# Kernel optimization log

Measured on AMD Instinct MI355X. Metric: run time of the kernel, lower is better.

Reference implementation:

```python
import jax, jax.numpy as jnp
import numpy as np

EMB = 512
HEAD = 8
HEAD_DIM = EMB // HEAD


def setup_inputs() -> dict:
    key = jax.random.key(0)
    ks = jax.random.split(key, 12)
    B, S = 2, 4096
    scale = 1.0 / np.sqrt(EMB)
    inp = {
        "q": jax.random.normal(ks[0], (B, S, EMB), dtype=jnp.float32),
        "kv": jax.random.normal(ks[1], (B, S, EMB), dtype=jnp.float32),
        "Wq": jax.random.normal(ks[2], (EMB, EMB), dtype=jnp.float32) * scale,
        "bq": jax.random.normal(ks[3], (EMB,), dtype=jnp.float32) * 0.01,
        "Wk": jax.random.normal(ks[4], (EMB, EMB), dtype=jnp.float32) * scale,
        "bk": jax.random.normal(ks[5], (EMB,), dtype=jnp.float32) * 0.01,
        "Wv": jax.random.normal(ks[6], (EMB, EMB), dtype=jnp.float32) * scale,
        "bv": jax.random.normal(ks[7], (EMB,), dtype=jnp.float32) * 0.01,
        "Wo": jax.random.normal(ks[8], (EMB, EMB), dtype=jnp.float32) * scale,
        "bo": jax.random.normal(ks[9], (EMB,), dtype=jnp.float32) * 0.01,
    }
    return inp


def reference(q, kv, Wq, bq, Wk, bk, Wv, bv, Wo, bo):
    B, N, _ = q.shape
    M = kv.shape[1]
    # Linear projections (torch Linear: x @ W^T + b)
    qh = (q @ Wq.T + bq).reshape(B, N, HEAD, HEAD_DIM).transpose(0, 2, 1, 3)  # [B,H,N,d]
    kh = (kv @ Wk.T + bk).reshape(B, M, HEAD, HEAD_DIM).transpose(0, 2, 1, 3)  # [B,H,M,d]
    vh = (kv @ Wv.T + bv).reshape(B, M, HEAD, HEAD_DIM).transpose(0, 2, 1, 3)  # [B,H,M,d]
    attn = jnp.einsum("bhnd,bhmd->bhnm", qh, kh) / jnp.sqrt(jnp.float32(HEAD_DIM))
    attn = jax.nn.softmax(attn, axis=-1)
    out = jnp.einsum("bhnm,bhmd->bhnd", attn, vh)  # [B,H,N,d]
    out = out.transpose(0, 2, 1, 3).reshape(B, N, EMB)
    out = out @ Wo.T + bo
    return out
```

## Files before the change

### kernel.cpp

```cpp
#include <hip/hip_runtime.h>
#include <stdint.h>

typedef unsigned short u16;
typedef __attribute__((ext_vector_type(8))) short short8;
typedef __attribute__((ext_vector_type(4))) float f32x4;
typedef __attribute__((ext_vector_type(16))) float f32x16;

typedef __attribute__((address_space(1))) void as1_void;
typedef __attribute__((address_space(3))) void as3_void;

__device__ inline u16 f2bf(float x) {
  uint32_t u = __float_as_uint(x);
  return (u16)((u + 0x7fffu + ((u >> 16) & 1u)) >> 16);
}

__device__ inline void gload16(const void* g, void* l) {
  __builtin_amdgcn_global_load_lds((as1_void*)g, (as3_void*)l, 16, 0, 0);
}

__device__ inline uint32_t cvtpk(float lo, float hi) {
  uint32_t d;
  asm("v_cvt_pk_bf16_f32 %0, %1, %2" : "=v"(d) : "v"(lo), "v"(hi));
  return d;
}

__device__ inline void plswap(uint32_t& a, uint32_t& b) {
  asm("v_permlane32_swap_b32 %0, %1" : "+v"(a), "+v"(b));
}

__device__ inline float fexp2(float x) {
  float r;
  asm("v_exp_f32 %0, %1" : "=v"(r) : "v"(x));
  return r;
}

__global__ __launch_bounds__(256) void cvt_all(const float* __restrict__ q,
                                               const float* __restrict__ kv,
                                               const float* __restrict__ Wq,
                                               const float* __restrict__ Wk,
                                               const float* __restrict__ Wv,
                                               const float* __restrict__ Wo,
                                               u16* __restrict__ qb,
                                               u16* __restrict__ kvb,
                                               u16* __restrict__ wall) {
  const int bx = blockIdx.x;
  const float* in;
  u16* out;
  int i;
  if (bx < 4096) {
    in = q; out = qb; i = bx * 256 + threadIdx.x;
  } else if (bx < 8192) {
    in = kv; out = kvb; i = (bx - 4096) * 256 + threadIdx.x;
  } else {
    int widx = (bx - 8192) >> 8;
    in = (widx == 0) ? Wq : (widx == 1) ? Wk : (widx == 2) ? Wv : Wo;
    out = wall + (size_t)widx * 262144;
    i = ((bx - 8192) & 255) * 256 + threadIdx.x;
  }
  float4 v = ((const float4*)in)[i];
  ushort4 o;
  o.x = f2bf(v.x); o.y = f2bf(v.y); o.z = f2bf(v.z); o.w = f2bf(v.w);
  ((ushort4*)out)[i] = o;
}

__global__ __launch_bounds__(256) void gemm_qkv(const u16* __restrict__ qb,
                                                const u16* __restrict__ kvb,
                                                const u16* __restrict__ wq,
                                                const u16* __restrict__ wk,
                                                const u16* __restrict__ wv,
                                                const float* __restrict__ bq,
                                                const float* __restrict__ bk,
                                                const float* __restrict__ bv,
                                                u16* __restrict__ Qh,
                                                u16* __restrict__ Kh,
                                                u16* __restrict__ Vt, float qscale) {
  __shared__ __align__(16) char smem[49152];
  const int z = blockIdx.z;
  const u16* A = (z == 0) ? qb : kvb;
  const u16* W = (z == 0) ? wq : (z == 1) ? wk : wv;
  const float* bias = (z == 0) ? bq : (z == 1) ? bk : bv;
  const float prescale = (z == 0) ? qscale : 1.0f;
  u16* Cout = (z == 0) ? Qh : (z == 1) ? Kh : Vt;

  const int tid = threadIdx.x;
  const int lane = tid & 63;
  const int wv_ = tid >> 6;
  const int c = lane & 15;
  const int g = lane >> 4;
  const int wr = wv_ >> 1, wc = wv_ & 1;
  const int m0 = blockIdx.x * 64;
  const int n0 = blockIdx.y * 128;

  const int r0 = tid >> 3, cc = tid & 7;
  const int u0 = cc ^ (r0 & 7);
  const u16* srcA0 = A + (size_t)(m0 + r0) * 512 + u0 * 8;
  const u16* srcW0 = W + (size_t)(n0 + r0) * 512 + u0 * 8;

#define GEMM_STAGE(BUF, KK)                              \
  {                                                      \
    char* ab_ = (char*)smem + (BUF)*24576 + wv_ * 1024;  \
    gload16(srcA0 + (KK), ab_);                          \
    gload16(srcA0 + (KK) + 16384, ab_ + 4096);           \
    gload16(srcW0 + (KK), ab_ + 8192);                   \
    gload16(srcW0 + (KK) + 16384, ab_ + 12288);          \
    gload16(srcW0 + (KK) + 32768, ab_ + 16384);          \
    gload16(srcW0 + (KK) + 49152, ab_ + 20480);          \
  }

  f32x4 acc[2][4];
#pragma unroll
  for (int i = 0; i < 2; i++)
#pragma unroll
    for (int j = 0; j < 4; j++) acc[i][j] = (f32x4){0.f, 0.f, 0.f, 0.f};

  GEMM_STAGE(0, 0)
  __syncthreads();
  int cur = 0;
  const int swa = c & 7;
  for (int it = 0; it < 8; ++it) {
    if (it < 7) GEMM_STAGE(cur ^ 1, (it + 1) * 64)
    const u16* Ab = (const u16*)((char*)smem + cur * 24576);
    const u16* Wb = Ab + 4096;
#pragma unroll
    for (int kd = 0; kd < 2; kd++) {
      short8 af[2], wf[4];
#pragma unroll
      for (int ai = 0; ai < 2; ai++)
        af[ai] = *(const short8*)&Ab[(wr * 32 + ai * 16 + c) * 64 + (((kd * 4 + g) ^ swa) << 3)];
#pragma unroll
      for (int bj = 0; bj < 4; bj++)
        wf[bj] = *(const short8*)&Wb[(wc * 64 + bj * 16 + c) * 64 + (((kd * 4 + g) ^ swa) << 3)];
#pragma unroll
      for (int ai = 0; ai < 2; ai++)
#pragma unroll
        for (int bj = 0; bj < 4; bj++)
          acc[ai][bj] = __builtin_amdgcn_mfma_f32_16x16x32_bf16(af[ai], wf[bj], acc[ai][bj], 0, 0, 0);
    }
    __syncthreads();
    cur ^= 1;
  }

#pragma unroll
  for (int ai = 0; ai < 2; ai++)
#pragma unroll
    for (int bj = 0; bj < 4; bj++)
#pragma unroll
      for (int r = 0; r < 4; r++) {
        int m = m0 + wr * 32 + ai * 16 + g * 4 + r;
        int n = n0 + wc * 64 + bj * 16 + c;
        float v = (acc[ai][bj][r] + bias[n]) * prescale;
        int b = m >> 12, s = m & 4095;
        int h = n >> 6, d = n & 63;
        size_t idx;
        if (z < 2)
          idx = ((size_t)(b * 8 + h) * 4096 + s) * 64 + d;
        else
          idx = ((size_t)(b * 8 + h) * 64 + d) * 4096 + s;
        Cout[idx] = f2bf(v);
      }
}

__global__ __launch_bounds__(256) void gemm_out(const u16* __restrict__ A,
                                                const u16* __restrict__ W,
                                                const float* __restrict__ bias,
                                                float* __restrict__ Cout) {
  __shared__ __align__(16) char smem[49152];
  const int tid = threadIdx.x;
  const int lane = tid & 63;
  const int wv_ = tid >> 6;
  const int c = lane & 15;
  const int g = lane >> 4;
  const int wr = wv_ >> 1, wc = wv_ & 1;
  const int m0 = blockIdx.x * 64;
  const int n0 = blockIdx.y * 128;

  const int r0 = tid >> 3, cc = tid & 7;
  const int u0 = cc ^ (r0 & 7);
  const u16* srcA0 = A + (size_t)(m0 + r0) * 512 + u0 * 8;
  const u16* srcW0 = W + (size_t)(n0 + r0) * 512 + u0 * 8;

  f32x4 acc[2][4];
#pragma unroll
  for (int i = 0; i < 2; i++)
#pragma unroll
    for (int j = 0; j < 4; j++) acc[i][j] = (f32x4){0.f, 0.f, 0.f, 0.f};

  GEMM_STAGE(0, 0)
  __syncthreads();
  int cur = 0;
  const int swa = c & 7;
  for (int it = 0; it < 8; ++it) {
    if (it < 7) GEMM_STAGE(cur ^ 1, (it + 1) * 64)
    const u16* Ab = (const u16*)((char*)smem + cur * 24576);
    const u16* Wb = Ab + 4096;
#pragma unroll
    for (int kd = 0; kd < 2; kd++) {
      short8 af[2], wf[4];
#pragma unroll
      for (int ai = 0; ai < 2; ai++)
        af[ai] = *(const short8*)&Ab[(wr * 32 + ai * 16 + c) * 64 + (((kd * 4 + g) ^ swa) << 3)];
#pragma unroll
      for (int bj = 0; bj < 4; bj++)
        wf[bj] = *(const short8*)&Wb[(wc * 64 + bj * 16 + c) * 64 + (((kd * 4 + g) ^ swa) << 3)];
#pragma unroll
      for (int ai = 0; ai < 2; ai++)
#pragma unroll
        for (int bj = 0; bj < 4; bj++)
          acc[ai][bj] = __builtin_amdgcn_mfma_f32_16x16x32_bf16(af[ai], wf[bj], acc[ai][bj], 0, 0, 0);
    }
    __syncthreads();
    cur ^= 1;
  }

#pragma unroll
  for (int ai = 0; ai < 2; ai++)
#pragma unroll
    for (int bj = 0; bj < 4; bj++)
#pragma unroll
      for (int r = 0; r < 4; r++) {
        int m = m0 + wr * 32 + ai * 16 + g * 4 + r;
        int n = n0 + wc * 64 + bj * 16 + c;
        Cout[(size_t)m * 512 + n] = acc[ai][bj][r] + bias[n];
      }
}

__global__ __launch_bounds__(256) void attn_split(const u16* __restrict__ Qh,
                                                  const u16* __restrict__ Kh,
                                                  const u16* __restrict__ Vt,
                                                  float* __restrict__ Op,
                                                  float* __restrict__ Lw) {
  __shared__ __align__(16) char smem[32768];
  const int tid = threadIdx.x;
  const int lane = tid & 63;
  const int w = tid >> 6;
  const int c5 = lane & 31;
  const int h = lane >> 5;
  const int bid = (blockIdx.x & 7) * 128 + (blockIdx.x >> 3);
  const int half = bid & 1;
  const int qt = (bid >> 1) & 31;
  const int bh = bid >> 6;
  const int q0 = qt * 128 + w * 32;
  const u16* Qb = Qh + (size_t)bh * 262144;
  const u16* Kb = Kh + (size_t)bh * 262144 + (size_t)half * 2048 * 64;
  const u16* Vb = Vt + (size_t)bh * 262144 + half * 2048;

  short8 qf[4];
#pragma unroll
  for (int kd = 0; kd < 4; kd++)
    qf[kd] = *(const short8*)(Qb + (size_t)(q0 + c5) * 64 + kd * 16 + h * 8);

  f32x16 accO[2];
#pragma unroll
  for (int i = 0; i < 16; i++) { accO[0][i] = 0.f; accO[1][i] = 0.f; }
  float l_loc = 0.f;

  const int r = tid >> 4, p = tid & 15;
  const int x = p ^ r;
  const int gb = x >> 3, ge = x & 7;
  const u16* srcKA = Kb + (size_t)(r + 32 * gb) * 64 + ge * 8;
  const u16* srcKB = Kb + (size_t)(16 + r + 32 * gb) * 64 + ge * 8;
  const u16* srcVA = Vb + (size_t)(r + 32 * gb) * 4096 + ge * 8;
  const u16* srcVB = Vb + (size_t)(16 + r + 32 * gb) * 4096 + ge * 8;

#define ATTN_STAGE(BUF, T)                                \
  {                                                       \
    char* b_ = (char*)smem + (BUF)*16384 + w * 1024;      \
    gload16(srcKA + (size_t)(T)*4096, b_);                \
    gload16(srcKB + (size_t)(T)*4096, b_ + 4096);         \
    gload16(srcVA + (T)*64, b_ + 8192);                   \
    gload16(srcVB + (T)*64, b_ + 12288);                  \
  }

  ATTN_STAGE(0, 0)
  __syncthreads();
  const int swz = c5 & 15;
  const int rowb = c5 * 128;

  short8 pa_prev[4];
  short8 vf_prev[8];

  for (int t = 0; t < 32; ++t) {
    const int cur = t & 1;
    if (t < 31) ATTN_STAGE(cur ^ 1, t + 1)

    const u16* Kl = (const u16*)(smem + cur * 16384);
    const u16* Vl = Kl + 4096;

    f32x16 s0, s1;
#pragma unroll
    for (int i = 0; i < 16; i++) { s0[i] = 0.f; s1[i] = 0.f; }
    __builtin_amdgcn_s_setprio(1);
#pragma unroll
    for (int kd = 0; kd < 4; kd++) {
      short8 kf0 = *(const short8*)&Kl[rowb + ((((kd << 1) + h) ^ swz) << 3)];
      short8 kf1 = *(const short8*)&Kl[rowb + (((8 + (kd << 1) + h) ^ swz) << 3)];
      s0 = __builtin_amdgcn_mfma_f32_32x32x16_bf16(kf0, qf[kd], s0, 0, 0, 0);
      s1 = __builtin_amdgcn_mfma_f32_32x32x16_bf16(kf1, qf[kd], s1, 0, 0, 0);
    }
    if (t > 0) {
#pragma unroll
      for (int km = 0; km < 4; km++) {
        accO[0] = __builtin_amdgcn_mfma_f32_32x32x16_bf16(vf_prev[2 * km], pa_prev[km], accO[0], 0, 0, 0);
        accO[1] = __builtin_amdgcn_mfma_f32_32x32x16_bf16(vf_prev[2 * km + 1], pa_prev[km], accO[1], 0, 0, 0);
      }
    }
    __builtin_amdgcn_s_setprio(0);
    __builtin_amdgcn_sched_barrier(0);

#pragma unroll
    for (int i = 0; i < 16; i++) { s0[i] = fexp2(s0[i]); s1[i] = fexp2(s1[i]); }

    float tsum0 = ((s0[0] + s1[0]) + (s0[4] + s1[4])) + ((s0[8] + s1[8]) + (s0[12] + s1[12]));
    float tsum1 = ((s0[1] + s1[1]) + (s0[5] + s1[5])) + ((s0[9] + s1[9]) + (s0[13] + s1[13]));
    float tsum2 = ((s0[2] + s1[2]) + (s0[6] + s1[6])) + ((s0[10] + s1[10]) + (s0[14] + s1[14]));
    float tsum3 = ((s0[3] + s1[3]) + (s0[7] + s1[7])) + ((s0[11] + s1[11]) + (s0[15] + s1[15]));
    l_loc += (tsum0 + tsum1) + (tsum2 + tsum3);

    uint32_t pk0[4][2], pk1[4][2];
#pragma unroll
    for (int u = 0; u < 4; u++) {
      pk0[u][0] = cvtpk(s0[4 * u], s0[4 * u + 1]);
      pk0[u][1] = cvtpk(s0[4 * u + 2], s0[4 * u + 3]);
      pk1[u][0] = cvtpk(s1[4 * u], s1[4 * u + 1]);
      pk1[u][1] = cvtpk(s1[4 * u + 2], s1[4 * u + 3]);
    }
#pragma unroll
    for (int km = 0; km < 2; km++) {
      const int uA = (km & 1) * 2, uB = uA + 1;
      uint32_t a0 = pk0[uA][0], b0 = pk0[uB][0]; plswap(a0, b0);
      uint32_t a1 = pk0[uA][1], b1 = pk0[uB][1]; plswap(a1, b1);
      union { uint32_t u[4]; short8 s; } uu;
      uu.u[0] = a0; uu.u[1] = a1; uu.u[2] = b0; uu.u[3] = b1;
      pa_prev[km] = uu.s;
    }
#pragma unroll
    for (int km = 2; km < 4; km++) {
      const int uA = (km & 1) * 2, uB = uA + 1;
      uint32_t a0 = pk1[uA][0], b0 = pk1[uB][0]; plswap(a0, b0);
      uint32_t a1 = pk1[uA][1], b1 = pk1[uB][1]; plswap(a1, b1);
      union { uint32_t u[4]; short8 s; } uu;
      uu.u[0] = a0; uu.u[1] = a1; uu.u[2] = b0; uu.u[3] = b1;
      pa_prev[km] = uu.s;
    }

#pragma unroll
    for (int km = 0; km < 4; km++) {
      vf_prev[2 * km]     = *(const short8*)&Vl[rowb + ((((km << 1) + h) ^ swz) << 3)];
      vf_prev[2 * km + 1] = *(const short8*)&Vl[rowb + (((8 + (km << 1) + h) ^ swz) << 3)];
    }

    __syncthreads();
  }

#pragma unroll
  for (int km = 0; km < 4; km++) {
    accO[0] = __builtin_amdgcn_mfma_f32_32x32x16_bf16(vf_prev[2 * km], pa_prev[km], accO[0], 0, 0, 0);
    accO[1] = __builtin_amdgcn_mfma_f32_32x32x16_bf16(vf_prev[2 * km + 1], pa_prev[km], accO[1], 0, 0, 0);
  }
  const float l_r = l_loc + __shfl_xor(l_loc, 32);

  const size_t pbase = (size_t)(half * 16 + bh) * 4096 + q0 + c5;
  float* Opw = Op + pbase * 64;
#pragma unroll
  for (int db = 0; db < 2; db++)
#pragma unroll
    for (int rr = 0; rr < 16; rr++) {
      int d = db * 32 + 4 * h + (rr & 3) + 8 * (rr >> 2);
      Opw[d] = accO[db][rr];
    }
  if (h == 0) Lw[pbase] = l_r;
}

__global__ __launch_bounds__(256) void attn_combine(const float* __restrict__ Op,
                                                    const float* __restrict__ Lw,
                                                    u16* __restrict__ aO) {
  int tg = blockIdx.x * 256 + threadIdx.x;
  int bhq = tg >> 3, seg = tg & 7;
  const float* p0 = Op + (size_t)bhq * 64 + seg * 8;
  const float* p1 = p0 + 4194304;
  float inv = 1.f / (Lw[bhq] + Lw[65536 + bhq]);
  float4 x0 = ((const float4*)p0)[0], x1 = ((const float4*)p0)[1];
  float4 y0 = ((const float4*)p1)[0], y1 = ((const float4*)p1)[1];
  ushort4 o0, o1;
  o0.x = f2bf((x0.x + y0.x) * inv);
  o0.y = f2bf((x0.y + y0.y) * inv);
  o0.z = f2bf((x0.z + y0.z) * inv);
  o0.w = f2bf((x0.w + y0.w) * inv);
  o1.x = f2bf((x1.x + y1.x) * inv);
  o1.y = f2bf((x1.y + y1.y) * inv);
  o1.z = f2bf((x1.z + y1.z) * inv);
  o1.w = f2bf((x1.w + y1.w) * inv);
  int bh = bhq >> 12, q = bhq & 4095;
  int b = bh >> 3, hh = bh & 7;
  u16* dst = aO + ((size_t)(b * 4096 + q)) * 512 + hh * 64 + seg * 8;
  ((ushort4*)dst)[0] = o0;
  ((ushort4*)dst)[1] = o1;
}

extern "C" void kernel_launch(void* const* d_in, const int* in_sizes, int n_in,
                              void* d_out, int out_size, void* d_ws, size_t ws_size,
                              hipStream_t stream) {
  const float* q  = (const float*)d_in[0];
  const float* kv = (const float*)d_in[1];
  const float* Wq = (const float*)d_in[2];
  const float* bq = (const float*)d_in[3];
  const float* Wk = (const float*)d_in[4];
  const float* bk = (const float*)d_in[5];
  const float* Wv = (const float*)d_in[6];
  const float* bv = (const float*)d_in[7];
  const float* Wo = (const float*)d_in[8];
  const float* bo = (const float*)d_in[9];

  const size_t MB = 1u << 20;
  char* ws = (char*)d_ws;
  u16* qb  = (u16*)(ws + 0 * MB);
  u16* kvb = (u16*)(ws + 8 * MB);
  u16* wqb = (u16*)(ws + 16 * MB);
  u16* wkb = (u16*)(ws + 16 * MB + 524288);
  u16* wvb = (u16*)(ws + 17 * MB);
  u16* wob = (u16*)(ws + 17 * MB + 524288);
  u16* Qh  = (u16*)(ws + 18 * MB);
  u16* Kh  = (u16*)(ws + 26 * MB);
  u16* Vt  = (u16*)(ws + 34 * MB);
  u16* aO  = (u16*)(ws + 42 * MB);
  float* Op = (float*)(ws + 50 * MB);
  float* Lw = (float*)(ws + 84 * MB);

  cvt_all<<<dim3(9216), dim3(256), 0, stream>>>(q, kv, Wq, Wk, Wv, Wo, qb, kvb, wqb);

  const float qscale = 0.125f * 1.44269504088896340736f;
  gemm_qkv<<<dim3(128, 4, 3), dim3(256), 0, stream>>>(qb, kvb, wqb, wkb, wvb,
                                                      bq, bk, bv, Qh, Kh, Vt, qscale);

  attn_split<<<dim3(1024), dim3(256), 0, stream>>>(Qh, Kh, Vt, Op, Lw);
  attn_combine<<<dim3(2048), dim3(256), 0, stream>>>(Op, Lw, aO);

  gemm_out<<<dim3(128, 4), dim3(256), 0, stream>>>(aO, wob, bo, (float*)d_out);
}
```

Baseline: 140.1 us.

## Fuse activation bf16 conversion into QKV GEMM and split-combine into output GEMM

The QKV projection GEMM now reads fp32 q/kv directly, converts them to bf16 in registers and writes them to LDS, so the separate activation conversion pass and its intermediate buffers go away. The output GEMM likewise reads the two fp32 partial attention outputs and their row sums, normalizes them and converts to bf16 while staging its A tile, which removes the attn_combine kernel and the aO round trip. This saves two launches and several large global writes and reads. In exchange the GEMMs issue register-path fp32 loads, which are twice the bytes of the old bf16 A tiles, plus the conversion math. gemm_out also re-reads the partial outputs once for each of its four N-blocks.

```diff
diff --git a/kernel.cpp b/kernel.cpp
--- a/kernel.cpp
+++ b/kernel.cpp
@@ -34,37 +34,23 @@
   return r;
 }
 
-__global__ __launch_bounds__(256) void cvt_all(const float* __restrict__ q,
-                                               const float* __restrict__ kv,
-                                               const float* __restrict__ Wq,
-                                               const float* __restrict__ Wk,
-                                               const float* __restrict__ Wv,
-                                               const float* __restrict__ Wo,
-                                               u16* __restrict__ qb,
-                                               u16* __restrict__ kvb,
-                                               u16* __restrict__ wall) {
-  const int bx = blockIdx.x;
-  const float* in;
-  u16* out;
-  int i;
-  if (bx < 4096) {
-    in = q; out = qb; i = bx * 256 + threadIdx.x;
-  } else if (bx < 8192) {
-    in = kv; out = kvb; i = (bx - 4096) * 256 + threadIdx.x;
-  } else {
-    int widx = (bx - 8192) >> 8;
-    in = (widx == 0) ? Wq : (widx == 1) ? Wk : (widx == 2) ? Wv : Wo;
-    out = wall + (size_t)widx * 262144;
-    i = ((bx - 8192) & 255) * 256 + threadIdx.x;
-  }
+__global__ __launch_bounds__(256) void cvt_w(const float* __restrict__ Wq,
+                                             const float* __restrict__ Wk,
+                                             const float* __restrict__ Wv,
+                                             const float* __restrict__ Wo,
+                                             u16* __restrict__ wall) {
+  const int widx = blockIdx.x >> 8;
+  const float* in = (widx == 0) ? Wq : (widx == 1) ? Wk : (widx == 2) ? Wv : Wo;
+  u16* out = wall + (size_t)widx * 262144;
+  int i = (blockIdx.x & 255) * 256 + threadIdx.x;
   float4 v = ((const float4*)in)[i];
   ushort4 o;
   o.x = f2bf(v.x); o.y = f2bf(v.y); o.z = f2bf(v.z); o.w = f2bf(v.w);
   ((ushort4*)out)[i] = o;
 }
 
-__global__ __launch_bounds__(256) void gemm_qkv(const u16* __restrict__ qb,
-                                                const u16* __restrict__ kvb,
+__global__ __launch_bounds__(256) void gemm_qkv(const float* __restrict__ qf,
+                                                const float* __restrict__ kvf,
                                                 const u16* __restrict__ wq,
                                                 const u16* __restrict__ wk,
                                                 const u16* __restrict__ wv,
@@ -76,7 +62,7 @@
                                                 u16* __restrict__ Vt, float qscale) {
   __shared__ __align__(16) char smem[49152];
   const int z = blockIdx.z;
-  const u16* A = (z == 0) ? qb : kvb;
+  const float* Af = (z == 0) ? qf : kvf;
   const u16* W = (z == 0) ? wq : (z == 1) ? wk : wv;
   const float* bias = (z == 0) ? bq : (z == 1) ? bk : bv;
   const float prescale = (z == 0) ? qscale : 1.0f;
@@ -93,32 +79,57 @@
 
   const int r0 = tid >> 3, cc = tid & 7;
   const int u0 = cc ^ (r0 & 7);
-  const u16* srcA0 = A + (size_t)(m0 + r0) * 512 + u0 * 8;
+  const float* srcAf = Af + (size_t)(m0 + r0) * 512 + u0 * 8;
   const u16* srcW0 = W + (size_t)(n0 + r0) * 512 + u0 * 8;
 
-#define GEMM_STAGE(BUF, KK)                              \
+#define QKV_W_STAGE(BUF, KK)                             \
   {                                                      \
     char* ab_ = (char*)smem + (BUF)*24576 + wv_ * 1024;  \
-    gload16(srcA0 + (KK), ab_);                          \
-    gload16(srcA0 + (KK) + 16384, ab_ + 4096);           \
     gload16(srcW0 + (KK), ab_ + 8192);                   \
     gload16(srcW0 + (KK) + 16384, ab_ + 12288);          \
     gload16(srcW0 + (KK) + 32768, ab_ + 16384);          \
     gload16(srcW0 + (KK) + 49152, ab_ + 20480);          \
   }
 
+#define QKV_A_WRITE(BUF)                                          \
+  {                                                               \
+    union { uint32_t u[4]; int4 v; } w0_, w1_;                    \
+    w0_.u[0] = cvtpk(a0.x, a0.y); w0_.u[1] = cvtpk(a0.z, a0.w);   \
+    w0_.u[2] = cvtpk(a1.x, a1.y); w0_.u[3] = cvtpk(a1.z, a1.w);   \
+    w1_.u[0] = cvtpk(a2.x, a2.y); w1_.u[1] = cvtpk(a2.z, a2.w);   \
+    w1_.u[2] = cvtpk(a3.x, a3.y); w1_.u[3] = cvtpk(a3.z, a3.w);   \
+    char* db_ = (char*)smem + (BUF)*24576;                        \
+    *(int4*)(db_ + tid * 16) = w0_.v;                             \
+    *(int4*)(db_ + 4096 + tid * 16) = w1_.v;                      \
+  }
+
   f32x4 acc[2][4];
 #pragma unroll
   for (int i = 0; i < 2; i++)
 #pragma unroll
     for (int j = 0; j < 4; j++) acc[i][j] = (f32x4){0.f, 0.f, 0.f, 0.f};
 
-  GEMM_STAGE(0, 0)
+  {
+    QKV_W_STAGE(0, 0)
+    float4 a0 = *(const float4*)(srcAf);
+    float4 a1 = *(const float4*)(srcAf + 4);
+    float4 a2 = *(const float4*)(srcAf + 16384);
+    float4 a3 = *(const float4*)(srcAf + 16388);
+    QKV_A_WRITE(0)
+  }
   __syncthreads();
   int cur = 0;
   const int swa = c & 7;
   for (int it = 0; it < 8; ++it) {
-    if (it < 7) GEMM_STAGE(cur ^ 1, (it + 1) * 64)
+    float4 a0, a1, a2, a3;
+    if (it < 7) {
+      const int kn = (it + 1) * 64;
+      QKV_W_STAGE(cur ^ 1, kn)
+      a0 = *(const float4*)(srcAf + kn);
+      a1 = *(const float4*)(srcAf + kn + 4);
+      a2 = *(const float4*)(srcAf + kn + 16384);
+      a3 = *(const float4*)(srcAf + kn + 16388);
+    }
     const u16* Ab = (const u16*)((char*)smem + cur * 24576);
     const u16* Wb = Ab + 4096;
 #pragma unroll
@@ -136,6 +147,7 @@
         for (int bj = 0; bj < 4; bj++)
           acc[ai][bj] = __builtin_amdgcn_mfma_f32_16x16x32_bf16(af[ai], wf[bj], acc[ai][bj], 0, 0, 0);
     }
+    if (it < 7) QKV_A_WRITE(cur ^ 1)
     __syncthreads();
     cur ^= 1;
   }
@@ -160,7 +172,8 @@
       }
 }
 
-__global__ __launch_bounds__(256) void gemm_out(const u16* __restrict__ A,
+__global__ __launch_bounds__(256) void gemm_out(const float* __restrict__ Op,
+                                                const float* __restrict__ Lw,
                                                 const u16* __restrict__ W,
                                                 const float* __restrict__ bias,
                                                 float* __restrict__ Cout) {
@@ -176,21 +189,80 @@
 
   const int r0 = tid >> 3, cc = tid & 7;
   const int u0 = cc ^ (r0 & 7);
-  const u16* srcA0 = A + (size_t)(m0 + r0) * 512 + u0 * 8;
   const u16* srcW0 = W + (size_t)(n0 + r0) * 512 + u0 * 8;
 
+  const int b_blk = m0 >> 12;
+  const int sb = (m0 & 4095) + r0;
+  const float* srcO0 = Op + ((size_t)(b_blk * 8) * 4096 + sb) * 64 + u0 * 8;
+  const float* lw0 = Lw + (size_t)(b_blk * 8) * 4096 + sb;
+
+#define OUT_W_STAGE(BUF, KK)                             \
+  {                                                      \
+    char* ab_ = (char*)smem + (BUF)*24576 + wv_ * 1024;  \
+    gload16(srcW0 + (KK), ab_ + 8192);                   \
+    gload16(srcW0 + (KK) + 16384, ab_ + 12288);          \
+    gload16(srcW0 + (KK) + 32768, ab_ + 16384);          \
+    gload16(srcW0 + (KK) + 49152, ab_ + 20480);          \
+  }
+
+#define OUT_A_LOAD(HH)                                              \
+  {                                                                 \
+    const float* p_ = srcO0 + (size_t)(HH)*262144;                  \
+    x0 = *(const float4*)(p_);                                      \
+    x1 = *(const float4*)(p_ + 4);                                  \
+    x2 = *(const float4*)(p_ + 2048);                  \
+    x3 = *(const float4*)(p_ + 2052);                               \
+    y0 = *(const float4*)(p_ + 4194304);                            \
+    y1 = *(const float4*)(p_ + 4194308);                            \
+    y2 = *(const float4*)(p_ + 4196352);                            \
+    y3 = *(const float4*)(p_ + 4196356);                            \
+    float la0 = lw0[(size_t)(HH)*4096];                             \
+    float lb0 = lw0[65536 + (size_t)(HH)*4096];                     \
+    float la1 = lw0[(size_t)(HH)*4096 + 32];                        \
+    float lb1 = lw0[65536 + (size_t)(HH)*4096 + 32];                \
+    il0 = 1.0f / (la0 + lb0);                                       \
+    il1 = 1.0f / (la1 + lb1);                                       \
+  }
+
+#define OUT_A_WRITE(BUF)                                                        \
+  {                                                                             \
+    union { uint32_t u[4]; int4 v; } w0_, w1_;                                  \
+    w0_.u[0] = cvtpk((x0.x + y0.x) * il0, (x0.y + y0.y) * il0);                 \
+    w0_.u[1] = cvtpk((x0.z + y0.z) * il0, (x0.w + y0.w) * il0);                 \
+    w0_.u[2] = cvtpk((x1.x + y1.x) * il0, (x1.y + y1.y) * il0);                 \
+    w0_.u[3] = cvtpk((x1.z + y1.z) * il0, (x1.w + y1.w) * il0);                 \
+    w1_.u[0] = cvtpk((x2.x + y2.x) * il1, (x2.y + y2.y) * il1);                 \
+    w1_.u[1] = cvtpk((x2.z + y2.z) * il1, (x2.w + y2.w) * il1);                 \
+    w1_.u[2] = cvtpk((x3.x + y3.x) * il1, (x3.y + y3.y) * il1);                 \
+    w1_.u[3] = cvtpk((x3.z + y3.z) * il1, (x3.w + y3.w) * il1);                 \
+    char* db_ = (char*)smem + (BUF)*24576;                                      \
+    *(int4*)(db_ + tid * 16) = w0_.v;                                           \
+    *(int4*)(db_ + 4096 + tid * 16) = w1_.v;                                    \
+  }
+
   f32x4 acc[2][4];
 #pragma unroll
   for (int i = 0; i < 2; i++)
 #pragma unroll
     for (int j = 0; j < 4; j++) acc[i][j] = (f32x4){0.f, 0.f, 0.f, 0.f};
 
-  GEMM_STAGE(0, 0)
+  {
+    float4 x0, x1, x2, x3, y0, y1, y2, y3;
+    float il0, il1;
+    OUT_W_STAGE(0, 0)
+    OUT_A_LOAD(0)
+    OUT_A_WRITE(0)
+  }
   __syncthreads();
   int cur = 0;
   const int swa = c & 7;
   for (int it = 0; it < 8; ++it) {
-    if (it < 7) GEMM_STAGE(cur ^ 1, (it + 1) * 64)
+    float4 x0, x1, x2, x3, y0, y1, y2, y3;
+    float il0, il1;
+    if (it < 7) {
+      OUT_W_STAGE(cur ^ 1, (it + 1) * 64)
+      OUT_A_LOAD(it + 1)
+    }
     const u16* Ab = (const u16*)((char*)smem + cur * 24576);
     const u16* Wb = Ab + 4096;
 #pragma unroll
@@ -208,6 +280,7 @@
         for (int bj = 0; bj < 4; bj++)
           acc[ai][bj] = __builtin_amdgcn_mfma_f32_16x16x32_bf16(af[ai], wf[bj], acc[ai][bj], 0, 0, 0);
     }
+    if (it < 7) OUT_A_WRITE(cur ^ 1)
     __syncthreads();
     cur ^= 1;
   }
@@ -371,32 +444,6 @@
   if (h == 0) Lw[pbase] = l_r;
 }
 
-__global__ __launch_bounds__(256) void attn_combine(const float* __restrict__ Op,
-                                                    const float* __restrict__ Lw,
-                                                    u16* __restrict__ aO) {
-  int tg = blockIdx.x * 256 + threadIdx.x;
-  int bhq = tg >> 3, seg = tg & 7;
-  const float* p0 = Op + (size_t)bhq * 64 + seg * 8;
-  const float* p1 = p0 + 4194304;
-  float inv = 1.f / (Lw[bhq] + Lw[65536 + bhq]);
-  float4 x0 = ((const float4*)p0)[0], x1 = ((const float4*)p0)[1];
-  float4 y0 = ((const float4*)p1)[0], y1 = ((const float4*)p1)[1];
-  ushort4 o0, o1;
-  o0.x = f2bf((x0.x + y0.x) * inv);
-  o0.y = f2bf((x0.y + y0.y) * inv);
-  o0.z = f2bf((x0.z + y0.z) * inv);
-  o0.w = f2bf((x0.w + y0.w) * inv);
-  o1.x = f2bf((x1.x + y1.x) * inv);
-  o1.y = f2bf((x1.y + y1.y) * inv);
-  o1.z = f2bf((x1.z + y1.z) * inv);
-  o1.w = f2bf((x1.w + y1.w) * inv);
-  int bh = bhq >> 12, q = bhq & 4095;
-  int b = bh >> 3, hh = bh & 7;
-  u16* dst = aO + ((size_t)(b * 4096 + q)) * 512 + hh * 64 + seg * 8;
-  ((ushort4*)dst)[0] = o0;
-  ((ushort4*)dst)[1] = o1;
-}
-
 extern "C" void kernel_launch(void* const* d_in, const int* in_sizes, int n_in,
                               void* d_out, int out_size, void* d_ws, size_t ws_size,
                               hipStream_t stream) {
@@ -413,8 +460,6 @@
 
   const size_t MB = 1u << 20;
   char* ws = (char*)d_ws;
-  u16* qb  = (u16*)(ws + 0 * MB);
-  u16* kvb = (u16*)(ws + 8 * MB);
   u16* wqb = (u16*)(ws + 16 * MB);
   u16* wkb = (u16*)(ws + 16 * MB + 524288);
   u16* wvb = (u16*)(ws + 17 * MB);
@@ -422,18 +467,16 @@
   u16* Qh  = (u16*)(ws + 18 * MB);
   u16* Kh  = (u16*)(ws + 26 * MB);
   u16* Vt  = (u16*)(ws + 34 * MB);
-  u16* aO  = (u16*)(ws + 42 * MB);
   float* Op = (float*)(ws + 50 * MB);
   float* Lw = (float*)(ws + 84 * MB);
 
-  cvt_all<<<dim3(9216), dim3(256), 0, stream>>>(q, kv, Wq, Wk, Wv, Wo, qb, kvb, wqb);
+  cvt_w<<<dim3(1024), dim3(256), 0, stream>>>(Wq, Wk, Wv, Wo, wqb);
 
   const float qscale = 0.125f * 1.44269504088896340736f;
-  gemm_qkv<<<dim3(128, 4, 3), dim3(256), 0, stream>>>(qb, kvb, wqb, wkb, wvb,
+  gemm_qkv<<<dim3(128, 4, 3), dim3(256), 0, stream>>>(q, kv, wqb, wkb, wvb,
                                                       bq, bk, bv, Qh, Kh, Vt, qscale);
 
   attn_split<<<dim3(1024), dim3(256), 0, stream>>>(Qh, Kh, Vt, Op, Lw);
-  attn_combine<<<dim3(2048), dim3(256), 0, stream>>>(Op, Lw, aO);
-
-  gemm_out<<<dim3(128, 4), dim3(256), 0, stream>>>(aO, wob, bo, (float*)d_out);
-}
+
+  gemm_out<<<dim3(128, 4), dim3(256), 0, stream>>>(Op, Lw, wob, bo, (float*)d_out);
+}
```

Result: no change. 140.1 us (+0.0%).
